# Kernel optimization log

Hardware: AMD Instinct MI355X
Metric: run time of the kernel (lower is better)

## Reference

```python
import jax, jax.numpy as jnp
import numpy as np

D = 512
H = 8
DH = D // H
HID = int(2 * D * 4.0 * (2.0 / 3.0))  # 2730, SwiGLU hidden


def _ln(x, g, b, eps=1e-5):
    m = jnp.mean(x, axis=-1, keepdims=True)
    v = jnp.mean(jnp.square(x - m), axis=-1, keepdims=True)
    return (x - m) * jax.lax.rsqrt(v + eps) * g + b


def _cross_attn(q_tok, kv_tok, ln_q_g, ln_q_b, ln_kv_g, ln_kv_b,
                Wqkv, bqkv, Wo, bo, Wp, bp):
    # q_tok: [B,Nq,D], kv_tok: [B,Nk,D]; Wqkv: [3D,D] fused in_proj (torch layout)
    B, Nq, _ = q_tok.shape
    Nk = kv_tok.shape[1]
    qn = _ln(q_tok, ln_q_g, ln_q_b)
    kvn = _ln(kv_tok, ln_kv_g, ln_kv_b)
    Wq, Wk, Wv = Wqkv[:D], Wqkv[D:2 * D], Wqkv[2 * D:]
    bq, bk, bv = bqkv[:D], bqkv[D:2 * D], bqkv[2 * D:]
    q = (qn @ Wq.T + bq).reshape(B, Nq, H, DH).transpose(0, 2, 1, 3)
    k = (kvn @ Wk.T + bk).reshape(B, Nk, H, DH).transpose(0, 2, 1, 3)
    v = (kvn @ Wv.T + bv).reshape(B, Nk, H, DH).transpose(0, 2, 1, 3)
    scores = jnp.einsum('bhqd,bhkd->bhqk', q, k) / jnp.sqrt(jnp.asarray(DH, q.dtype))
    attn = jax.nn.softmax(scores, axis=-1)
    ctx = jnp.einsum('bhqk,bhkd->bhqd', attn, v)
    ctx = ctx.transpose(0, 2, 1, 3).reshape(B, Nq, D)
    ctx = ctx @ Wo.T + bo          # MHA out_proj
    ctx = ctx @ Wp.T + bp          # CrossAttention extra out_proj
    return q_tok + ctx             # residual (dropout/droppath identity in eval)


def setup_inputs() -> dict:
    key = jax.random.key(0)
    ks = iter(jax.random.split(key, 32))
    s = 0.02
    inp = {
        'spatial_tokens': jax.random.normal(next(ks), (4, 4096, D), jnp.float32),
        'temporal_tokens': jax.random.normal(next(ks), (4, 512, D), jnp.float32),
    }
    for p in ('s', 't'):
        inp[f'{p}_ln_q_g'] = jnp.ones((D,), jnp.float32)
        inp[f'{p}_ln_q_b'] = jnp.zeros((D,), jnp.float32)
        inp[f'{p}_ln_kv_g'] = jnp.ones((D,), jnp.float32)
        inp[f'{p}_ln_kv_b'] = jnp.zeros((D,), jnp.float32)
        inp[f'{p}_Wqkv'] = jax.random.normal(next(ks), (3 * D, D), jnp.float32) * s
        inp[f'{p}_bqkv'] = jnp.zeros((3 * D,), jnp.float32)
        inp[f'{p}_Wo'] = jax.random.normal(next(ks), (D, D), jnp.float32) * s
        inp[f'{p}_bo'] = jnp.zeros((D,), jnp.float32)
        inp[f'{p}_Wp'] = jax.random.normal(next(ks), (D, D), jnp.float32) * s
        inp[f'{p}_bp'] = jnp.zeros((D,), jnp.float32)
    inp['mix_ln_g'] = jnp.ones((2 * D,), jnp.float32)
    inp['mix_ln_b'] = jnp.zeros((2 * D,), jnp.float32)
    inp['mix_Win'] = jax.random.normal(next(ks), (2 * HID, 2 * D), jnp.float32) * s
    inp['mix_bin'] = jnp.zeros((2 * HID,), jnp.float32)
    inp['mix_Wout'] = jax.random.normal(next(ks), (D, HID), jnp.float32) * s
    inp['mix_bout'] = jnp.zeros((D,), jnp.float32)
    return inp


def reference(spatial_tokens, temporal_tokens,
              s_ln_q_g, s_ln_q_b, s_ln_kv_g, s_ln_kv_b, s_Wqkv, s_bqkv, s_Wo, s_bo, s_Wp, s_bp,
              t_ln_q_g, t_ln_q_b, t_ln_kv_g, t_ln_kv_b, t_Wqkv, t_bqkv, t_Wo, t_bo, t_Wp, t_bp,
              mix_ln_g, mix_ln_b, mix_Win, mix_bin, mix_Wout, mix_bout):
    # 'st' (spatiotemporal) mode of CrossTransformer.forward
    s_ctx = _cross_attn(spatial_tokens, temporal_tokens,
                        s_ln_q_g, s_ln_q_b, s_ln_kv_g, s_ln_kv_b,
                        s_Wqkv, s_bqkv, s_Wo, s_bo, s_Wp, s_bp)
    t_ctx = _cross_attn(temporal_tokens, spatial_tokens,
                        t_ln_q_g, t_ln_q_b, t_ln_kv_g, t_ln_kv_b,
                        t_Wqkv, t_bqkv, t_Wo, t_bo, t_Wp, t_bp)
    t_mean = jnp.mean(t_ctx, axis=1, keepdims=True)  # [B,1,D]
    base = jnp.concatenate([s_ctx, jnp.broadcast_to(t_mean, s_ctx.shape)], axis=-1)  # [B,Ns,2D]
    h = _ln(base, mix_ln_g, mix_ln_b)
    uv = h @ mix_Win.T + mix_bin            # [B,Ns,2*HID]
    u, v = uv[..., :HID], uv[..., HID:]
    fused = (jax.nn.silu(u) * v) @ mix_Wout.T + mix_bout
    return s_ctx + fused
```

## Files before the change

### kernel.cpp

```cpp
#include <hip/hip_runtime.h>
#include <stdint.h>

typedef unsigned short u16;
typedef __bf16 bf16_t;
typedef bf16_t bf16x8 __attribute__((ext_vector_type(8)));
typedef float f32x4 __attribute__((ext_vector_type(4)));

__device__ __forceinline__ u16 f2b(float f) {
  union { float f; uint32_t u; } x; x.f = f;
  uint32_t r = x.u + 0x7fffu + ((x.u >> 16) & 1u);
  return (u16)(r >> 16);
}
__device__ __forceinline__ float b2f(u16 b) {
  union { uint32_t u; float f; } x; x.u = ((uint32_t)b) << 16;
  return x.f;
}

__device__ __forceinline__ void async16(const void* g, void* l) {
  auto gp = reinterpret_cast<__attribute__((address_space(1))) unsigned int*>(
      reinterpret_cast<uintptr_t>(g));
  auto lp = reinterpret_cast<__attribute__((address_space(3))) unsigned int*>(
      reinterpret_cast<uintptr_t>(l));
  __builtin_amdgcn_global_load_lds(gp, lp, 16, 0, 0);
}

__global__ __launch_bounds__(256) void pz_gemm_bt(
    const u16* __restrict__ A, const u16* __restrict__ B,
    const float* __restrict__ bias,
    const u16* __restrict__ residB, const float* __restrict__ residF,
    u16* __restrict__ Cb, float* __restrict__ Cf,
    int M, int N, int K, int ldA, int ldB, int ldC, int ldR,
    long aSH, long bSH, long cSH, long rSH, float alpha)
{
  __shared__ __align__(16) u16 sA[2][128 * 32];
  __shared__ __align__(16) u16 sB[2][128 * 32];

  const int tid = threadIdx.x;
  const int wave = tid >> 6, lane = tid & 63;
  const int lr = lane & 15, lg = lane >> 4;
  const int wm = wave >> 1, wn = wave & 1;
  const int z = blockIdx.z;

  const u16* Ab = A + (long)z * aSH;
  const u16* Bb = B + (long)z * bSH;
  const int m0 = blockIdx.y * 128;
  const int n0 = blockIdx.x * 128;

  const int srow = tid >> 2;
  const int sgk = (tid & 3) ^ ((tid >> 3) & 3);
  int ar0 = m0 + srow;      if (ar0 > M - 1) ar0 = M - 1;
  int ar1 = m0 + 64 + srow; if (ar1 > M - 1) ar1 = M - 1;
  int br0 = n0 + srow;      if (br0 > N - 1) br0 = N - 1;
  int br1 = n0 + 64 + srow; if (br1 > N - 1) br1 = N - 1;
  const u16* aP0 = Ab + (long)ar0 * ldA + sgk * 8;
  const u16* aP1 = Ab + (long)ar1 * ldA + sgk * 8;
  const u16* bP0 = Bb + (long)br0 * ldB + sgk * 8;
  const u16* bP1 = Bb + (long)br1 * ldB + sgk * 8;

  auto stage = [&](int buf, int k0) {
    async16(aP0 + k0, sA[buf] + wave * 512);
    async16(aP1 + k0, sA[buf] + 2048 + wave * 512);
    async16(bP0 + k0, sB[buf] + wave * 512);
    async16(bP1 + k0, sB[buf] + 2048 + wave * 512);
  };

  const int swz = (lr >> 1) & 3;
  int aoff[4], boff[4];
#pragma unroll
  for (int i = 0; i < 4; ++i) {
    aoff[i] = (wm * 64 + i * 16 + lr) * 32 + ((lg ^ swz) * 8);
    boff[i] = (wn * 64 + i * 16 + lr) * 32 + ((lg ^ swz) * 8);
  }

  f32x4 acc[4][4] = {};
  const int kiters = K >> 5;

  stage(0, 0);
  __builtin_amdgcn_s_waitcnt(0x0f70);
  __syncthreads();

  int cur = 0;
  for (int kt = 0; kt < kiters; ++kt) {
    if (kt + 1 < kiters) stage(cur ^ 1, (kt + 1) << 5);

    const u16* sAc = sA[cur];
    const u16* sBc = sB[cur];
    bf16x8 af[4], bfr[4];
#pragma unroll
    for (int i = 0; i < 4; ++i) af[i] = *(const bf16x8*)(sAc + aoff[i]);
#pragma unroll
    for (int i = 0; i < 4; ++i) bfr[i] = *(const bf16x8*)(sBc + boff[i]);
#pragma unroll
    for (int i = 0; i < 4; ++i)
#pragma unroll
      for (int j = 0; j < 4; ++j)
        acc[i][j] = __builtin_amdgcn_mfma_f32_16x16x32_bf16(af[i], bfr[j], acc[i][j], 0, 0, 0);

    __builtin_amdgcn_s_waitcnt(0x0f70);
    __syncthreads();
    cur ^= 1;
  }

  const long coff = (long)z * cSH;
  const long roff = (long)z * rSH;
#pragma unroll
  for (int j = 0; j < 4; ++j) {
    const int n = n0 + wn * 64 + j * 16 + lr;
    if (n < N) {
      const float bv = bias ? bias[n] : 0.0f;
#pragma unroll
      for (int i = 0; i < 4; ++i) {
        const int mb = m0 + wm * 64 + i * 16 + lg * 4;
#pragma unroll
        for (int r = 0; r < 4; ++r) {
          const int m = mb + r;
          float v = alpha * acc[i][j][r] + bv;
          const long ri = roff + (long)m * ldR + n;
          if (residB) v += b2f(residB[ri]);
          if (residF) v += residF[ri];
          const long ci = coff + (long)m * ldC + n;
          if (Cb) Cb[ci] = f2b(v);
          if (Cf) Cf[ci] = v;
        }
      }
    }
  }
}

__global__ __launch_bounds__(256) void pz_sattn(
    const u16* __restrict__ Q, const u16* __restrict__ K,
    const u16* __restrict__ V, u16* __restrict__ O)
{
  __shared__ __align__(16) u16 sQ[32 * 64];
  __shared__ __align__(16) u16 sK[512 * 32];
  __shared__ float redm[32][4];
  __shared__ float reds[32][4];

  const int tid = threadIdx.x;
  const int wave = tid >> 6, lane = tid & 63;
  const int lr = lane & 15, lg = lane >> 4;
  const int z = blockIdx.z;
  const int b = z >> 3, h = z & 7;
  const int q0 = blockIdx.x * 32;

  const u16* Qb = Q + (long)b * 4096 * 512 + h * 64;
  const u16* Kb = K + (long)b * 512 * 1024 + h * 64;
  const u16* Vb = V + ((long)b * 8 + h) * (64L * 512);
  u16* Ob = O + (long)b * 4096 * 512 + h * 64;

  {
    const int qrow = wave * 8 + (lane >> 3);
    const int qcol = ((lane & 7) ^ (lane >> 3)) * 8;
    async16(Qb + (long)(q0 + qrow) * 512 + qcol, sQ + wave * 512);
  }
  const int krow = wave * 16 + (lane >> 2);
  const int kcol = ((lane & 3) ^ ((lane >> 3) & 3)) * 8;
  const u16* kP = Kb + (long)krow * 1024 + kcol;

  f32x4 acc[8][2] = {};
#pragma unroll
  for (int kk = 0; kk < 2; ++kk) {
    __syncthreads();
#pragma unroll
    for (int s = 0; s < 8; ++s)
      async16(kP + kk * 32 + (long)s * 64 * 1024, sK + s * 2048 + wave * 512);
    __builtin_amdgcn_s_waitcnt(0x0f70);
    __syncthreads();

    bf16x8 kf[8], qf[2];
#pragma unroll
    for (int kb = 0; kb < 8; ++kb) {
      const int n = wave * 128 + kb * 16 + lr;
      kf[kb] = *(const bf16x8*)(sK + n * 32 + ((lg ^ ((lr >> 1) & 3)) * 8));
    }
#pragma unroll
    for (int nq = 0; nq < 2; ++nq) {
      const int r = nq * 16 + lr;
      qf[nq] = *(const bf16x8*)(sQ + r * 64 + (((kk * 4 + lg) ^ (r & 7)) * 8));
    }
#pragma unroll
    for (int kb = 0; kb < 8; ++kb)
#pragma unroll
      for (int nq = 0; nq < 2; ++nq)
        acc[kb][nq] = __builtin_amdgcn_mfma_f32_16x16x32_bf16(kf[kb], qf[nq], acc[kb][nq], 0, 0, 0);
  }

  float mx0, mx1;
  {
    float m0 = acc[0][0][0], m1 = acc[0][1][0];
#pragma unroll
    for (int kb = 0; kb < 8; ++kb)
#pragma unroll
      for (int rg = 0; rg < 4; ++rg) {
        m0 = fmaxf(m0, acc[kb][0][rg]);
        m1 = fmaxf(m1, acc[kb][1][rg]);
      }
    m0 = fmaxf(m0, __shfl_xor(m0, 16, 64)); m0 = fmaxf(m0, __shfl_xor(m0, 32, 64));
    m1 = fmaxf(m1, __shfl_xor(m1, 16, 64)); m1 = fmaxf(m1, __shfl_xor(m1, 32, 64));
    mx0 = m0; mx1 = m1;
  }
  if (lane < 16) { redm[lr][wave] = mx0; redm[16 + lr][wave] = mx1; }
  __syncthreads();
  float inv[2];
#pragma unroll
  for (int nq = 0; nq < 2; ++nq) {
    const int q = nq * 16 + lr;
    const float m = fmaxf(fmaxf(redm[q][0], redm[q][1]), fmaxf(redm[q][2], redm[q][3]));
    float s = 0.0f;
#pragma unroll
    for (int kb = 0; kb < 8; ++kb)
#pragma unroll
      for (int rg = 0; rg < 4; ++rg) {
        const float e = __expf(0.125f * (acc[kb][nq][rg] - m));
        acc[kb][nq][rg] = e;
        s += e;
      }
    s += __shfl_xor(s, 16, 64);
    s += __shfl_xor(s, 32, 64);
    if (lane < 16) reds[q][wave] = s;
  }
  __syncthreads();
#pragma unroll
  for (int nq = 0; nq < 2; ++nq) {
    const int q = nq * 16 + lr;
    inv[nq] = 1.0f / (reds[q][0] + reds[q][1] + reds[q][2] + reds[q][3]);
  }

#pragma unroll
  for (int nq = 0; nq < 2; ++nq) {
    const int q = nq * 16 + lr;
#pragma unroll
    for (int kb = 0; kb < 8; ++kb) {
      ushort4 w;
      w.x = f2b(acc[kb][nq][0] * inv[nq]);
      w.y = f2b(acc[kb][nq][1] * inv[nq]);
      w.z = f2b(acc[kb][nq][2] * inv[nq]);
      w.w = f2b(acc[kb][nq][3] * inv[nq]);
      const int c16 = wave * 16 + kb * 2 + (lg >> 1);
      const int byteoff = q * 1024 + ((c16 ^ (q & 7)) * 16) + (lg & 1) * 8;
      *(ushort4*)((char*)sK + byteoff) = w;
    }
  }
  __syncthreads();

  const u16* vp = Vb + (long)(wave * 16 + lr) * 512;
  f32x4 opv[2] = {};
#pragma unroll
  for (int ks = 0; ks < 16; ++ks) {
    const bf16x8 bv = *(const bf16x8*)(vp + ks * 32 + lg * 8);
    bf16x8 pf[2];
#pragma unroll
    for (int mi = 0; mi < 2; ++mi) {
      const int r = mi * 16 + lr;
      pf[mi] = *(const bf16x8*)((char*)sK + r * 1024 + (((ks * 4 + lg) ^ (lr & 7)) * 16));
    }
#pragma unroll
    for (int mi = 0; mi < 2; ++mi)
      opv[mi] = __builtin_amdgcn_mfma_f32_16x16x32_bf16(pf[mi], bv, opv[mi], 0, 0, 0);
  }
#pragma unroll
  for (int mi = 0; mi < 2; ++mi)
#pragma unroll
    for (int rg = 0; rg < 4; ++rg) {
      const int q = q0 + mi * 16 + lg * 4 + rg;
      Ob[(long)q * 512 + wave * 16 + lr] = f2b(opv[mi][rg]);
    }
}

__global__ __launch_bounds__(256) void pz_tattn(
    const u16* __restrict__ Q,
    const u16* __restrict__ K,
    const u16* __restrict__ VT,
    u16* __restrict__ O)
{
  __shared__ __align__(16) u16 sQ[32 * 64];
  __shared__ __align__(16) u16 sK[512 * 32];
  __shared__ float redm[32][4];
  __shared__ float reds[32][4];
  __shared__ float m_run[32], l_run[32], alpha_sh[32];

  const int tid = threadIdx.x;
  const int wave = tid >> 6, lane = tid & 63;
  const int lr = lane & 15, lg = lane >> 4;
  const int z = blockIdx.z;
  const int b = z >> 3, h = z & 7;
  const int q0 = blockIdx.x * 32;

  const u16* Qb = Q + (long)b * 512 * 512 + h * 64;
  const u16* Kb = K + (long)b * 4096 * 1024 + h * 64;
  const u16* Vb = VT + (long)b * 512 * 4096 + (long)h * 64 * 4096;
  u16* Ob = O + (long)b * 512 * 512 + h * 64;

  if (tid < 32) { m_run[tid] = -3.0e38f; l_run[tid] = 0.0f; }

  {
    const int qrow = wave * 8 + (lane >> 3);
    const int qcol = ((lane & 7) ^ (lane >> 3)) * 8;
    async16(Qb + (long)(q0 + qrow) * 512 + qcol, sQ + wave * 512);
  }
  const int krow = wave * 16 + (lane >> 2);
  const int kcol = ((lane & 3) ^ ((lane >> 3) & 3)) * 8;

  f32x4 opv[2] = {};

  for (int kt = 0; kt < 8; ++kt) {
    const u16* kP = Kb + ((long)kt * 512 + krow) * 1024 + kcol;
    f32x4 acc[8][2] = {};
#pragma unroll
    for (int kk = 0; kk < 2; ++kk) {
      __syncthreads();
#pragma unroll
      for (int s = 0; s < 8; ++s)
        async16(kP + kk * 32 + (long)s * 64 * 1024, sK + s * 2048 + wave * 512);
      __builtin_amdgcn_s_waitcnt(0x0f70);
      __syncthreads();

      bf16x8 kf[8], qf[2];
#pragma unroll
      for (int kb = 0; kb < 8; ++kb) {
        const int n = wave * 128 + kb * 16 + lr;
        kf[kb] = *(const bf16x8*)(sK + n * 32 + ((lg ^ ((lr >> 1) & 3)) * 8));
      }
#pragma unroll
      for (int nq = 0; nq < 2; ++nq) {
        const int r = nq * 16 + lr;
        qf[nq] = *(const bf16x8*)(sQ + r * 64 + (((kk * 4 + lg) ^ (r & 7)) * 8));
      }
#pragma unroll
      for (int kb = 0; kb < 8; ++kb)
#pragma unroll
        for (int nq = 0; nq < 2; ++nq)
          acc[kb][nq] = __builtin_amdgcn_mfma_f32_16x16x32_bf16(kf[kb], qf[nq], acc[kb][nq], 0, 0, 0);
    }

#pragma unroll
    for (int nq = 0; nq < 2; ++nq) {
      float m = acc[0][nq][0];
#pragma unroll
      for (int kb = 0; kb < 8; ++kb)
#pragma unroll
        for (int rg = 0; rg < 4; ++rg) m = fmaxf(m, acc[kb][nq][rg]);
      m = fmaxf(m, __shfl_xor(m, 16, 64));
      m = fmaxf(m, __shfl_xor(m, 32, 64));
      if (lane < 16) redm[nq * 16 + lr][wave] = m;
    }
    __syncthreads();

#pragma unroll
    for (int nq = 0; nq < 2; ++nq) {
      const int q = nq * 16 + lr;
      const float mt = fmaxf(fmaxf(redm[q][0], redm[q][1]), fmaxf(redm[q][2], redm[q][3]));
      const float mn = fmaxf(m_run[q], mt);
      float s = 0.0f;
#pragma unroll
      for (int kb = 0; kb < 8; ++kb)
#pragma unroll
        for (int rg = 0; rg < 4; ++rg) {
          const float e = __expf(0.125f * (acc[kb][nq][rg] - mn));
          acc[kb][nq][rg] = e;
          s += e;
        }
      s += __shfl_xor(s, 16, 64);
      s += __shfl_xor(s, 32, 64);
      if (lane < 16) reds[q][wave] = s;
    }
    __syncthreads();

    if (tid < 32) {
      const int q = tid;
      const float mt = fmaxf(fmaxf(redm[q][0], redm[q][1]), fmaxf(redm[q][2], redm[q][3]));
      const float mo = m_run[q];
      const float mn = fmaxf(mo, mt);
      const float al = __expf(0.125f * (mo - mn));
      l_run[q] = l_run[q] * al + (reds[q][0] + reds[q][1] + reds[q][2] + reds[q][3]);
      m_run[q] = mn;
      alpha_sh[q] = al;
    }
#pragma unroll
    for (int nq = 0; nq < 2; ++nq) {
      const int q = nq * 16 + lr;
#pragma unroll
      for (int kb = 0; kb < 8; ++kb) {
        ushort4 w;
        w.x = f2b(acc[kb][nq][0]);
        w.y = f2b(acc[kb][nq][1]);
        w.z = f2b(acc[kb][nq][2]);
        w.w = f2b(acc[kb][nq][3]);
        const int c16 = wave * 16 + kb * 2 + (lg >> 1);
        const int byteoff = q * 1024 + ((c16 ^ (q & 7)) * 16) + (lg & 1) * 8;
        *(ushort4*)((char*)sK + byteoff) = w;
      }
    }
    __syncthreads();

#pragma unroll
    for (int mi = 0; mi < 2; ++mi)
#pragma unroll
      for (int rg = 0; rg < 4; ++rg)
        opv[mi][rg] *= alpha_sh[mi * 16 + lg * 4 + rg];

    const u16* vp = Vb + (long)(wave * 16 + lr) * 4096 + kt * 512;
#pragma unroll
    for (int ks = 0; ks < 16; ++ks) {
      const bf16x8 bv = *(const bf16x8*)(vp + ks * 32 + lg * 8);
      bf16x8 pf[2];
#pragma unroll
      for (int mi = 0; mi < 2; ++mi) {
        const int r = mi * 16 + lr;
        pf[mi] = *(const bf16x8*)((char*)sK + r * 1024 + (((ks * 4 + lg) ^ (lr & 7)) * 16));
      }
#pragma unroll
      for (int mi = 0; mi < 2; ++mi)
        opv[mi] = __builtin_amdgcn_mfma_f32_16x16x32_bf16(pf[mi], bv, opv[mi], 0, 0, 0);
    }
  }

#pragma unroll
  for (int mi = 0; mi < 2; ++mi)
#pragma unroll
    for (int rg = 0; rg < 4; ++rg) {
      const int qr = mi * 16 + lg * 4 + rg;
      Ob[(long)(q0 + qr) * 512 + wave * 16 + lr] = f2b(opv[mi][rg] * (1.0f / l_run[qr]));
    }
}

__global__ __launch_bounds__(256) void pz_gemm_uvgate(
    const u16* __restrict__ A, const u16* __restrict__ Bu, const u16* __restrict__ Bv,
    const float* __restrict__ biasU, const float* __restrict__ biasV,
    u16* __restrict__ G, int M, int N, int K, int ldA, int ldB, int ldG, int Npad)
{
  __shared__ __align__(16) u16 sAll[3 * 8192];

  const int tid = threadIdx.x;
  const int wave = tid >> 6, lane = tid & 63;
  const int lr = lane & 15, lg = lane >> 4;
  const int wm = wave >> 1, wn = wave & 1;
  const int m0 = blockIdx.y * 128;
  const int n0 = blockIdx.x * 64;

  const int srow = tid >> 2;
  const int sgk = (tid & 3) ^ ((tid >> 3) & 3);
  int ar0 = m0 + srow;      if (ar0 > M - 1) ar0 = M - 1;
  int ar1 = m0 + 64 + srow; if (ar1 > M - 1) ar1 = M - 1;
  int br  = n0 + srow;      if (br  > N - 1) br  = N - 1;
  const u16* aP0 = A + (long)ar0 * ldA + sgk * 8;
  const u16* aP1 = A + (long)ar1 * ldA + sgk * 8;
  const u16* uP  = Bu + (long)br * ldB + sgk * 8;
  const u16* vP  = Bv + (long)br * ldB + sgk * 8;

  auto stage = [&](int buf, int k0) {
    u16* b = sAll + buf * 8192;
    async16(aP0 + k0, b + wave * 512);
    async16(aP1 + k0, b + 2048 + wave * 512);
    async16(uP + k0, b + 4096 + wave * 512);
    async16(vP + k0, b + 6144 + wave * 512);
  };

  const int swz = (lr >> 1) & 3;
  int aoff[4], boff[2];
#pragma unroll
  for (int i = 0; i < 4; ++i) aoff[i] = (wm * 64 + i * 16 + lr) * 32 + ((lg ^ swz) * 8);
#pragma unroll
  for (int j = 0; j < 2; ++j) boff[j] = (wn * 32 + j * 16 + lr) * 32 + ((lg ^ swz) * 8);

  f32x4 aU[4][2] = {}, aV[4][2] = {};
  const int kiters = K >> 5;

  stage(0, 0);
  if (kiters > 1) stage(1, 32);

  int cur = 0;
  for (int kt = 0; kt < kiters; ++kt) {
    if (kt + 2 < kiters) {
      const int nx = (cur + 2 >= 3) ? cur - 1 : cur + 2;
      stage(nx, (kt + 2) << 5);
    }
    if (kt + 2 < kiters)      asm volatile("s_waitcnt vmcnt(8)" ::: "memory");
    else if (kt + 1 < kiters) asm volatile("s_waitcnt vmcnt(4)" ::: "memory");
    else                      asm volatile("s_waitcnt vmcnt(0)" ::: "memory");
    __builtin_amdgcn_s_barrier();
    asm volatile("" ::: "memory");

    const u16* base = sAll + cur * 8192;
    bf16x8 af[4], uf[2], vf[2];
#pragma unroll
    for (int i = 0; i < 4; ++i) af[i] = *(const bf16x8*)(base + aoff[i]);
#pragma unroll
    for (int j = 0; j < 2; ++j) uf[j] = *(const bf16x8*)(base + 4096 + boff[j]);
#pragma unroll
    for (int j = 0; j < 2; ++j) vf[j] = *(const bf16x8*)(base + 6144 + boff[j]);
#pragma unroll
    for (int i = 0; i < 4; ++i)
#pragma unroll
      for (int j = 0; j < 2; ++j) {
        aU[i][j] = __builtin_amdgcn_mfma_f32_16x16x32_bf16(af[i], uf[j], aU[i][j], 0, 0, 0);
        aV[i][j] = __builtin_amdgcn_mfma_f32_16x16x32_bf16(af[i], vf[j], aV[i][j], 0, 0, 0);
      }

    asm volatile("" ::: "memory");
    __builtin_amdgcn_s_barrier();
    cur = (cur + 1 == 3) ? 0 : cur + 1;
  }

#pragma unroll
  for (int j = 0; j < 2; ++j) {
    const int n = n0 + wn * 32 + j * 16 + lr;
    if (n < N) {
      const float bu = biasU[n], bv = biasV[n];
#pragma unroll
      for (int i = 0; i < 4; ++i) {
        const int mb = m0 + wm * 64 + i * 16 + lg * 4;
#pragma unroll
        for (int r = 0; r < 4; ++r) {
          const float u = aU[i][j][r] + bu;
          const float v = aV[i][j][r] + bv;
          G[(long)(mb + r) * ldG + n] = f2b((u / (1.0f + __expf(-u))) * v);
        }
      }
    } else if (n < Npad) {
#pragma unroll
      for (int i = 0; i < 4; ++i) {
        const int mb = m0 + wm * 64 + i * 16 + lg * 4;
#pragma unroll
        for (int r = 0; r < 4; ++r) G[(long)(mb + r) * ldG + n] = 0;
      }
    }
  }
}

__global__ __launch_bounds__(256) void pz_ln(const float* __restrict__ X, u16* __restrict__ O)
{
  __shared__ float sm[4], sq[4];
  const int tid = threadIdx.x;
  const long row = blockIdx.x;
  const float* x = X + row * 512;
  float a = x[tid], b = x[tid + 256];
  float s = a + b, q = a * a + b * b;
#pragma unroll
  for (int m = 32; m >= 1; m >>= 1) { s += __shfl_xor(s, m, 64); q += __shfl_xor(q, m, 64); }
  if ((tid & 63) == 0) { sm[tid >> 6] = s; sq[tid >> 6] = q; }
  __syncthreads();
  s = sm[0] + sm[1] + sm[2] + sm[3];
  q = sq[0] + sq[1] + sq[2] + sq[3];
  const float mean = s * (1.0f / 512.0f);
  const float rstd = rsqrtf(q * (1.0f / 512.0f) - mean * mean + 1e-5f);
  O[row * 512 + tid]       = f2b((a - mean) * rstd);
  O[row * 512 + tid + 256] = f2b((b - mean) * rstd);
}

__global__ __launch_bounds__(256) void pz_mix_ln(
    const u16* __restrict__ SC, const float* __restrict__ TM,
    const float* __restrict__ g, const float* __restrict__ b, u16* __restrict__ H)
{
  __shared__ float sm[4], sq[4];
  const int tid = threadIdx.x;
  const long row = blockIdx.x;
  const int bb = (int)(row >> 12);
  const u16* x0 = SC + row * 512;
  const float* x1 = TM + (long)bb * 512;
  float v0 = b2f(x0[tid]), v1 = b2f(x0[tid + 256]);
  float v2 = x1[tid], v3 = x1[tid + 256];
  float s = v0 + v1 + v2 + v3;
  float q = v0 * v0 + v1 * v1 + v2 * v2 + v3 * v3;
#pragma unroll
  for (int m = 32; m >= 1; m >>= 1) { s += __shfl_xor(s, m, 64); q += __shfl_xor(q, m, 64); }
  if ((tid & 63) == 0) { sm[tid >> 6] = s; sq[tid >> 6] = q; }
  __syncthreads();
  s = sm[0] + sm[1] + sm[2] + sm[3];
  q = sq[0] + sq[1] + sq[2] + sq[3];
  const float mean = s * (1.0f / 1024.0f);
  const float rstd = rsqrtf(q * (1.0f / 1024.0f) - mean * mean + 1e-5f);
  u16* hr = H + row * 1024;
  hr[tid]       = f2b((v0 - mean) * rstd * g[tid]       + b[tid]);
  hr[tid + 256] = f2b((v1 - mean) * rstd * g[tid + 256] + b[tid + 256]);
  hr[tid + 512] = f2b((v2 - mean) * rstd * g[tid + 512] + b[tid + 512]);
  hr[tid + 768] = f2b((v3 - mean) * rstd * g[tid + 768] + b[tid + 768]);
}

__global__ __launch_bounds__(256) void pz_transpose(
    const u16* __restrict__ S, u16* __restrict__ D, int Nk, int ldS, int colBase)
{
  __shared__ u16 t[64][65];
  const int z = blockIdx.z;
  const int nk0 = blockIdx.x * 64;
  const int tid = threadIdx.x;
  for (int i = tid; i < 4096; i += 256) {
    int r = i >> 6, d = i & 63;
    t[r][d] = S[(long)(nk0 + r) * ldS + colBase + z * 64 + d];
  }
  __syncthreads();
  for (int i = tid; i < 4096; i += 256) {
    int d = i >> 6, c = i & 63;
    D[((long)z * 64 + d) * Nk + nk0 + c] = t[c][d];
  }
}

__global__ __launch_bounds__(256) void pz_transpose_f2b(
    const float* __restrict__ S, u16* __restrict__ D, int Nk, int ldS)
{
  __shared__ u16 t[64][65];
  const int z = blockIdx.z;
  const int nk0 = blockIdx.x * 64;
  const int tid = threadIdx.x;
  for (int i = tid; i < 4096; i += 256) {
    int r = i >> 6, d = i & 63;
    t[r][d] = f2b(S[(long)(nk0 + r) * ldS + z * 64 + d]);
  }
  __syncthreads();
  for (int i = tid; i < 4096; i += 256) {
    int d = i >> 6, c = i & 63;
    D[((long)z * 64 + d) * Nk + nk0 + c] = t[c][d];
  }
}

__global__ __launch_bounds__(256) void pz_f2b(const float* __restrict__ s, u16* __restrict__ d, int n)
{
  int i = blockIdx.x * 256 + threadIdx.x;
  if (i < n) d[i] = f2b(s[i]);
}

__global__ __launch_bounds__(256) void pz_fold_qkv(
    const float* __restrict__ Ws, const float* __restrict__ Wt,
    const float* __restrict__ bs, const float* __restrict__ bt,
    const float* s_qg, const float* s_qb, const float* s_kg, const float* s_kb,
    const float* t_qg, const float* t_qb, const float* t_kg, const float* t_kb,
    u16* __restrict__ Wps, u16* __restrict__ Wpt, float* bps, float* bpt)
{
  __shared__ float sb[4];
  const int id = blockIdx.x;
  const int mat = (id >= 1536) ? 1 : 0;
  const int r = id - mat * 1536;
  const float* W = mat ? Wt : Ws;
  const float* bq = mat ? bt : bs;
  const float *g, *bl;
  if (!mat) { g = (r < 512) ? s_qg : s_kg; bl = (r < 512) ? s_qb : s_kb; }
  else      { g = (r < 512) ? t_qg : t_kg; bl = (r < 512) ? t_qb : t_kb; }
  u16* Wo_ = mat ? Wpt : Wps;
  float* bo_ = mat ? bpt : bps;
  float dot = 0.0f;
  for (int c = threadIdx.x; c < 512; c += 256) {
    float w = W[(long)r * 512 + c];
    Wo_[(long)r * 512 + c] = f2b(w * g[c]);
    dot += w * bl[c];
  }
#pragma unroll
  for (int m = 32; m >= 1; m >>= 1) dot += __shfl_xor(dot, m, 64);
  if ((threadIdx.x & 63) == 0) sb[threadIdx.x >> 6] = dot;
  __syncthreads();
  if (threadIdx.x == 0) bo_[r] = sb[0] + sb[1] + sb[2] + sb[3] + bq[r];
}

__global__ __launch_bounds__(256) void pz_fold_bc(
    const float* Wps_, const float* bos, const float* bps_,
    const float* Wpt_, const float* bot, const float* bpt_, float* bcs, float* bct)
{
  __shared__ float sb[4];
  const int id = blockIdx.x;
  const int mat = id >> 9, i = id & 511;
  const float* W = mat ? Wpt_ : Wps_;
  const float* bo = mat ? bot : bos;
  const float* bp = mat ? bpt_ : bps_;
  float* o = mat ? bct : bcs;
  float dot = 0.0f;
  for (int j = threadIdx.x; j < 512; j += 256) dot += W[(long)i * 512 + j] * bo[j];
#pragma unroll
  for (int m = 32; m >= 1; m >>= 1) dot += __shfl_xor(dot, m, 64);
  if ((threadIdx.x & 63) == 0) sb[threadIdx.x >> 6] = dot;
  __syncthreads();
  if (threadIdx.x == 0) o[i] = sb[0] + sb[1] + sb[2] + sb[3] + bp[i];
}

__global__ __launch_bounds__(256) void pz_pad_wout(const float* __restrict__ W, u16* __restrict__ D)
{
  const int idx = blockIdx.x * 256 + threadIdx.x;
  const int r = idx / 2816, c = idx - r * 2816;
  D[idx] = (c < 2730) ? f2b(W[(long)r * 2730 + c]) : (u16)0;
}

__global__ __launch_bounds__(256) void pz_tmean(const u16* __restrict__ T, float* __restrict__ O)
{
  const int b = blockIdx.y, tc = blockIdx.x, tid = threadIdx.x;
  const u16* base = T + (long)b * 512 * 512 + (long)tc * 32 * 512;
  float s0 = 0.0f, s1 = 0.0f;
#pragma unroll 4
  for (int t = 0; t < 32; ++t) { s0 += b2f(base[t * 512 + tid]); s1 += b2f(base[t * 512 + tid + 256]); }
  atomicAdd(&O[b * 512 + tid],       s0 * (1.0f / 512.0f));
  atomicAdd(&O[b * 512 + tid + 256], s1 * (1.0f / 512.0f));
}

__global__ void pz_diag(float* __restrict__ out, long n, float val)
{
  for (long i = (long)blockIdx.x * 256 + threadIdx.x; i < n; i += (long)gridDim.x * 256)
    out[i] = val;
}

extern "C" void kernel_launch(void* const* d_in, const int* in_sizes, int n_in,
                              void* d_out, int out_size, void* d_ws, size_t ws_size,
                              hipStream_t stream)
{
  (void)in_sizes; (void)n_in;
  const float* spat   = (const float*)d_in[0];
  const float* temp   = (const float*)d_in[1];
  const float* s_qg = (const float*)d_in[2],  * s_qb = (const float*)d_in[3];
  const float* s_kg = (const float*)d_in[4],  * s_kb = (const float*)d_in[5];
  const float* s_Wqkv = (const float*)d_in[6], * s_bqkv = (const float*)d_in[7];
  const float* s_Wo = (const float*)d_in[8],  * s_bo = (const float*)d_in[9];
  const float* s_Wp = (const float*)d_in[10], * s_bp = (const float*)d_in[11];
  const float* t_qg = (const float*)d_in[12], * t_qb = (const float*)d_in[13];
  const float* t_kg = (const float*)d_in[14], * t_kb = (const float*)d_in[15];
  const float* t_Wqkv = (const float*)d_in[16], * t_bqkv = (const float*)d_in[17];
  const float* t_Wo = (const float*)d_in[18], * t_bo = (const float*)d_in[19];
  const float* t_Wp = (const float*)d_in[20], * t_bp = (const float*)d_in[21];
  const float* mix_g = (const float*)d_in[22], * mix_b = (const float*)d_in[23];
  const float* mix_Win = (const float*)d_in[24], * mix_bin = (const float*)d_in[25];
  const float* mix_Wout = (const float*)d_in[26], * mix_bout = (const float*)d_in[27];
  float* out = (float*)d_out;

  char* ws = (char*)d_ws;
  size_t off = 0;
  auto take = [&](size_t n) { void* p = ws + off; off += (n + 255) & ~(size_t)255; return p; };

  u16* wq_s  = (u16*)take(1536L * 512 * 2);
  u16* wq_t  = (u16*)take(1536L * 512 * 2);
  u16* wc_s  = (u16*)take(512L * 512 * 2);
  u16* wc_t  = (u16*)take(512L * 512 * 2);
  u16* woutp = (u16*)take(512L * 2816 * 2);
  float* bqs = (float*)take(1536L * 4);
  float* bqt = (float*)take(1536L * 4);
  float* bcs = (float*)take(512L * 4);
  float* bct = (float*)take(512L * 4);
  u16* nhat_s = (u16*)take(16384L * 512 * 2);
  u16* nhat_t = (u16*)take(2048L * 512 * 2);
  u16* q_s  = (u16*)take(16384L * 512 * 2);
  u16* kv_s = (u16*)take(2048L * 1024 * 2);
  u16* q_t  = (u16*)take(2048L * 512 * 2);
  u16* kv_t = (u16*)take(16384L * 1024 * 2);
  char* Sreg = (char*)take(16777216 + 2097152 + 4194304);
  const size_t NEED = off;

  if (ws_size < NEED) {
    pz_diag<<<2048, 256, 0, stream>>>(out, (long)out_size, (float)(ws_size >> 20));
    return;
  }

  u16* Gbig = (u16*)(ws + off);
  const bool bigG = (ws_size >= off + 16384UL * 2816 * 2);

  u16* wtT  = (u16*)Sreg;
  u16* wpb  = (u16*)(Sreg + 524288);
  u16* vt_s = (u16*)Sreg;
  u16* vtc4 = (u16*)(Sreg + 2097152);
  u16* ctx_s = nhat_s;
  u16* ctx_t = nhat_t;
  u16* sctx  = q_s;
  u16* tctx  = kv_s;
  float* tmean = (float*)q_t;
  u16* hbuf  = kv_t;
  u16* gchunk = (u16*)Sreg;
  u16* winb   = (u16*)nhat_s;

  auto gemm = [&](const u16* A, const u16* B, const float* bias,
                  const u16* residB, const float* residF, u16* Cb, float* Cf,
                  int M, int N, int K, int ldA, int ldB, int ldC, int ldR,
                  long aSH, long bSH, long cSH, long rSH, int Z, float alpha) {
    dim3 g((N + 127) / 128, M / 128, Z);
    pz_gemm_bt<<<g, dim3(256), 0, stream>>>(A, B, bias, residB, residF, Cb, Cf,
        M, N, K, ldA, ldB, ldC, ldR, aSH, bSH, cSH, rSH, alpha);
  };

  pz_fold_qkv<<<3072, 256, 0, stream>>>(s_Wqkv, t_Wqkv, s_bqkv, t_bqkv,
      s_qg, s_qb, s_kg, s_kb, t_qg, t_qb, t_kg, t_kb, wq_s, wq_t, bqs, bqt);
  pz_transpose_f2b<<<dim3(8, 1, 8), 256, 0, stream>>>(s_Wo, wtT, 512, 512);
  pz_f2b<<<1024, 256, 0, stream>>>(s_Wp, wpb, 512 * 512);
  gemm(wpb, wtT, nullptr, nullptr, nullptr, wc_s, nullptr,
       512, 512, 512, 512, 512, 512, 0, 0, 0, 0, 0, 1, 1.0f);
  pz_transpose_f2b<<<dim3(8, 1, 8), 256, 0, stream>>>(t_Wo, wtT, 512, 512);
  pz_f2b<<<1024, 256, 0, stream>>>(t_Wp, wpb, 512 * 512);
  gemm(wpb, wtT, nullptr, nullptr, nullptr, wc_t, nullptr,
       512, 512, 512, 512, 512, 512, 0, 0, 0, 0, 0, 1, 1.0f);
  pz_fold_bc<<<1024, 256, 0, stream>>>(s_Wp, s_bo, s_bp, t_Wp, t_bo, t_bp, bcs, bct);
  pz_pad_wout<<<5632, 256, 0, stream>>>(mix_Wout, woutp);

  pz_ln<<<16384, 256, 0, stream>>>(spat, nhat_s);
  pz_ln<<<2048, 256, 0, stream>>>(temp, nhat_t);

  gemm(nhat_s, wq_s,           bqs,       nullptr, nullptr, q_s,  nullptr,
       16384, 512,  512, 512, 512, 512,  0, 0,0,0,0, 1, 1.0f);
  gemm(nhat_t, wq_s + 512*512, bqs + 512, nullptr, nullptr, kv_s, nullptr,
       2048,  1024, 512, 512, 512, 1024, 0, 0,0,0,0, 1, 1.0f);
  gemm(nhat_t, wq_t,           bqt,       nullptr, nullptr, q_t,  nullptr,
       2048,  512,  512, 512, 512, 512,  0, 0,0,0,0, 1, 1.0f);
  gemm(nhat_s, wq_t + 512*512, bqt + 512, nullptr, nullptr, kv_t, nullptr,
       16384, 1024, 512, 512, 512, 1024, 0, 0,0,0,0, 1, 1.0f);

  for (int b = 0; b < 4; ++b)
    pz_transpose<<<dim3(8, 1, 8), 256, 0, stream>>>(kv_s + (long)b * 512 * 1024,
        vt_s + (long)b * 8 * 64 * 512, 512, 1024, 512);
  for (int b = 0; b < 4; ++b)
    pz_transpose<<<dim3(64, 1, 8), 256, 0, stream>>>(kv_t + (long)b * 4096 * 1024,
        vtc4 + (long)b * 512 * 4096, 4096, 1024, 512);

  pz_sattn<<<dim3(128, 1, 32), 256, 0, stream>>>(q_s, kv_s, vt_s, ctx_s);
  pz_tattn<<<dim3(16, 1, 32), 256, 0, stream>>>(q_t, kv_t, vtc4, ctx_t);

  gemm(ctx_s, wc_s, bcs, nullptr, spat, sctx, nullptr,
       16384, 512, 512, 512, 512, 512, 512, 0,0,0,0, 1, 1.0f);
  gemm(ctx_t, wc_t, bct, nullptr, temp, tctx, nullptr,
       2048,  512, 512, 512, 512, 512, 512, 0,0,0,0, 1, 1.0f);

  (void)hipMemsetAsync(tmean, 0, 4L * 512 * sizeof(float), stream);
  pz_tmean<<<dim3(16, 4), 256, 0, stream>>>(tctx, tmean);
  pz_mix_ln<<<16384, 256, 0, stream>>>(sctx, tmean, mix_g, mix_b, hbuf);

  pz_f2b<<<21840, 256, 0, stream>>>(mix_Win, winb, 5460 * 1024);

  if (bigG) {
    pz_gemm_uvgate<<<dim3(44, 128), 256, 0, stream>>>(hbuf, winb, winb + 2730L * 1024,
        mix_bin, mix_bin + 2730, Gbig, 16384, 2730, 1024, 1024, 1024, 2816, 2816);
    gemm(Gbig, woutp, mix_bout, sctx, nullptr, nullptr, out,
         16384, 512, 2816, 2816, 2816, 512, 512, 0,0,0,0, 1, 1.0f);
  } else {
    for (int c = 0; c < 4; ++c) {
      const u16* Ah = hbuf + (long)c * 4096 * 1024;
      pz_gemm_uvgate<<<dim3(44, 32), 256, 0, stream>>>(Ah, winb, winb + 2730L * 1024,
          mix_bin, mix_bin + 2730, gchunk, 4096, 2730, 1024, 1024, 1024, 2816, 2816);
      gemm(gchunk, woutp, mix_bout, sctx + (long)c * 4096 * 512, nullptr, nullptr,
           out + (long)c * 4096 * 512,
           4096, 512, 2816, 2816, 2816, 512, 512, 0,0,0,0, 1, 1.0f);
    }
  }
}
```

Before: 871.0 us.

## Triple-buffer GEMM loads, raise MFMA priority in attention, batch transpose launches

The shared GEMM kernel moves from double to triple buffering of async global-to-LDS loads. Its waits become explicit vmcnt levels so loads run two k-steps ahead, and it needs one barrier fewer per iteration. The attention kernels wrap their MFMA blocks in s_setprio to favour matrix issue over other waves. The per-batch transpose launches are folded into one launch each using a batch grid dimension. Triple buffering raises LDS use per block, which may cut occupancy, and hand-written vmcnt counts depend on exactly four loads per stage.

```diff
diff --git a/kernel.cpp b/kernel.cpp
--- a/kernel.cpp
+++ b/kernel.cpp
@@ -32,8 +32,7 @@
     int M, int N, int K, int ldA, int ldB, int ldC, int ldR,
     long aSH, long bSH, long cSH, long rSH, float alpha)
 {
-  __shared__ __align__(16) u16 sA[2][128 * 32];
-  __shared__ __align__(16) u16 sB[2][128 * 32];
+  __shared__ __align__(16) u16 sAll[3 * 8192];
 
   const int tid = threadIdx.x;
   const int wave = tid >> 6, lane = tid & 63;
@@ -58,10 +57,11 @@
   const u16* bP1 = Bb + (long)br1 * ldB + sgk * 8;
 
   auto stage = [&](int buf, int k0) {
-    async16(aP0 + k0, sA[buf] + wave * 512);
-    async16(aP1 + k0, sA[buf] + 2048 + wave * 512);
-    async16(bP0 + k0, sB[buf] + wave * 512);
-    async16(bP1 + k0, sB[buf] + 2048 + wave * 512);
+    u16* p = sAll + buf * 8192;
+    async16(aP0 + k0, p + wave * 512);
+    async16(aP1 + k0, p + 2048 + wave * 512);
+    async16(bP0 + k0, p + 4096 + wave * 512);
+    async16(bP1 + k0, p + 6144 + wave * 512);
   };
 
   const int swz = (lr >> 1) & 3;
@@ -76,29 +76,35 @@
   const int kiters = K >> 5;
 
   stage(0, 0);
-  __builtin_amdgcn_s_waitcnt(0x0f70);
-  __syncthreads();
+  if (kiters > 1) stage(1, 32);
 
   int cur = 0;
   for (int kt = 0; kt < kiters; ++kt) {
-    if (kt + 1 < kiters) stage(cur ^ 1, (kt + 1) << 5);
-
-    const u16* sAc = sA[cur];
-    const u16* sBc = sB[cur];
+    if (kt + 2 < kiters) {
+      const int nx = (cur + 2 >= 3) ? cur - 1 : cur + 2;
+      stage(nx, (kt + 2) << 5);
+    }
+    if (kt + 2 < kiters)      asm volatile("s_waitcnt vmcnt(8)" ::: "memory");
+    else if (kt + 1 < kiters) asm volatile("s_waitcnt vmcnt(4)" ::: "memory");
+    else                      asm volatile("s_waitcnt vmcnt(0)" ::: "memory");
+    __builtin_amdgcn_s_barrier();
+    asm volatile("" ::: "memory");
+
+    const u16* base = sAll + cur * 8192;
     bf16x8 af[4], bfr[4];
 #pragma unroll
-    for (int i = 0; i < 4; ++i) af[i] = *(const bf16x8*)(sAc + aoff[i]);
-#pragma unroll
-    for (int i = 0; i < 4; ++i) bfr[i] = *(const bf16x8*)(sBc + boff[i]);
+    for (int i = 0; i < 4; ++i) af[i] = *(const bf16x8*)(base + aoff[i]);
+#pragma unroll
+    for (int i = 0; i < 4; ++i) bfr[i] = *(const bf16x8*)(base + 4096 + boff[i]);
 #pragma unroll
     for (int i = 0; i < 4; ++i)
 #pragma unroll
       for (int j = 0; j < 4; ++j)
         acc[i][j] = __builtin_amdgcn_mfma_f32_16x16x32_bf16(af[i], bfr[j], acc[i][j], 0, 0, 0);
 
-    __builtin_amdgcn_s_waitcnt(0x0f70);
-    __syncthreads();
-    cur ^= 1;
+    asm volatile("" ::: "memory");
+    __builtin_amdgcn_s_barrier();
+    cur = (cur + 1 == 3) ? 0 : cur + 1;
   }
 
   const long coff = (long)z * cSH;
@@ -178,11 +184,13 @@
       const int r = nq * 16 + lr;
       qf[nq] = *(const bf16x8*)(sQ + r * 64 + (((kk * 4 + lg) ^ (r & 7)) * 8));
     }
+    __builtin_amdgcn_s_setprio(1);
 #pragma unroll
     for (int kb = 0; kb < 8; ++kb)
 #pragma unroll
       for (int nq = 0; nq < 2; ++nq)
         acc[kb][nq] = __builtin_amdgcn_mfma_f32_16x16x32_bf16(kf[kb], qf[nq], acc[kb][nq], 0, 0, 0);
+    __builtin_amdgcn_s_setprio(0);
   }
 
   float mx0, mx1;
@@ -254,9 +262,11 @@
       const int r = mi * 16 + lr;
       pf[mi] = *(const bf16x8*)((char*)sK + r * 1024 + (((ks * 4 + lg) ^ (lr & 7)) * 16));
     }
+    __builtin_amdgcn_s_setprio(1);
 #pragma unroll
     for (int mi = 0; mi < 2; ++mi)
       opv[mi] = __builtin_amdgcn_mfma_f32_16x16x32_bf16(pf[mi], bv, opv[mi], 0, 0, 0);
+    __builtin_amdgcn_s_setprio(0);
   }
 #pragma unroll
   for (int mi = 0; mi < 2; ++mi)
@@ -326,11 +336,13 @@
         const int r = nq * 16 + lr;
         qf[nq] = *(const bf16x8*)(sQ + r * 64 + (((kk * 4 + lg) ^ (r & 7)) * 8));
       }
+      __builtin_amdgcn_s_setprio(1);
 #pragma unroll
       for (int kb = 0; kb < 8; ++kb)
 #pragma unroll
         for (int nq = 0; nq < 2; ++nq)
           acc[kb][nq] = __builtin_amdgcn_mfma_f32_16x16x32_bf16(kf[kb], qf[nq], acc[kb][nq], 0, 0, 0);
+      __builtin_amdgcn_s_setprio(0);
     }
 
 #pragma unroll
@@ -409,9 +421,11 @@
         const int r = mi * 16 + lr;
         pf[mi] = *(const bf16x8*)((char*)sK + r * 1024 + (((ks * 4 + lg) ^ (lr & 7)) * 16));
       }
+      __builtin_amdgcn_s_setprio(1);
 #pragma unroll
       for (int mi = 0; mi < 2; ++mi)
         opv[mi] = __builtin_amdgcn_mfma_f32_16x16x32_bf16(pf[mi], bv, opv[mi], 0, 0, 0);
+      __builtin_amdgcn_s_setprio(0);
     }
   }
 
@@ -578,12 +592,15 @@
 }
 
 __global__ __launch_bounds__(256) void pz_transpose(
-    const u16* __restrict__ S, u16* __restrict__ D, int Nk, int ldS, int colBase)
+    const u16* __restrict__ S, u16* __restrict__ D, int Nk, int ldS, int colBase,
+    long sBS, long dBS)
 {
   __shared__ u16 t[64][65];
   const int z = blockIdx.z;
   const int nk0 = blockIdx.x * 64;
   const int tid = threadIdx.x;
+  S += (long)blockIdx.y * sBS;
+  D += (long)blockIdx.y * dBS;
   for (int i = tid; i < 4096; i += 256) {
     int r = i >> 6, d = i & 63;
     t[r][d] = S[(long)(nk0 + r) * ldS + colBase + z * 64 + d];
@@ -793,12 +810,10 @@
   gemm(nhat_s, wq_t + 512*512, bqt + 512, nullptr, nullptr, kv_t, nullptr,
        16384, 1024, 512, 512, 512, 1024, 0, 0,0,0,0, 1, 1.0f);
 
-  for (int b = 0; b < 4; ++b)
-    pz_transpose<<<dim3(8, 1, 8), 256, 0, stream>>>(kv_s + (long)b * 512 * 1024,
-        vt_s + (long)b * 8 * 64 * 512, 512, 1024, 512);
-  for (int b = 0; b < 4; ++b)
-    pz_transpose<<<dim3(64, 1, 8), 256, 0, stream>>>(kv_t + (long)b * 4096 * 1024,
-        vtc4 + (long)b * 512 * 4096, 4096, 1024, 512);
+  pz_transpose<<<dim3(8, 4, 8), 256, 0, stream>>>(kv_s, vt_s, 512, 1024, 512,
+      512L * 1024, 8L * 64 * 512);
+  pz_transpose<<<dim3(64, 4, 8), 256, 0, stream>>>(kv_t, vtc4, 4096, 1024, 512,
+      4096L * 1024, 512L * 4096);
 
   pz_sattn<<<dim3(128, 1, 32), 256, 0, stream>>>(q_s, kv_s, vt_s, ctx_s);
   pz_tattn<<<dim3(16, 1, 32), 256, 0, stream>>>(q_t, kv_t, vtc4, ctx_t);
```

New measurement: 841.7 us. 3.4% less time.
